# Kernel tuning notes

Hardware: AMD Instinct MI355X
Metric: run time of the kernel (lower is better)

The kernel has to match this reference:

```python
import jax, jax.numpy as jnp
import numpy as np

NUM_HEADS = 16
EPS = 1e-15


def setup_inputs() -> dict:
    key = jax.random.key(0)
    k1, k2, k3, k4 = jax.random.split(key, 4)
    B, N, C = 4, 16384, 512
    x = jax.random.normal(k1, (B, N, C), dtype=jnp.float32)
    qkv_weight = jax.random.normal(k2, (3 * C, C), dtype=jnp.float32) * 0.02
    proj_weight = jax.random.normal(k3, (C, C), dtype=jnp.float32) * 0.02
    proj_bias = jax.random.normal(k4, (C,), dtype=jnp.float32) * 0.02
    return {"x": x, "qkv_weight": qkv_weight, "proj_weight": proj_weight, "proj_bias": proj_bias}


def reference(x, qkv_weight, proj_weight, proj_bias):
    B, N, C = x.shape
    H = NUM_HEADS
    D = C // H
    # fused linear + ReLU on q,k (v stays linear, per backward: grad_v has no relu mask)
    qkv = (x @ qkv_weight.T).reshape(B, N, 3, C)
    q = jax.nn.relu(qkv[:, :, 0]).reshape(B, N, H, D)
    k = jax.nn.relu(qkv[:, :, 1]).reshape(B, N, H, D)
    v = qkv[:, :, 2].reshape(B, N, H, D)
    qf = q.astype(jnp.float32)
    kf = k.astype(jnp.float32)
    vf = v.astype(jnp.float32)
    # pad v with a ones column -> normalizer row in vk (pad_vk_mm_fwd)
    v_pad = jnp.concatenate([vf, jnp.ones_like(vf[..., :1])], axis=-1)  # [B,N,H,D+1]
    vk = jnp.einsum('bnhc,bnhd->bhcd', v_pad, kf)  # [B,H,D+1,D] accumulated in fp32
    vk_q = jnp.einsum('bnhd,bhcd->bnhc', qf, vk)  # [B,N,H,D+1]
    # fused division by normalizer (vk_q_mm_divide_fwd)
    proj_input = (vk_q[..., :-1] / (vk_q[..., -1:] + EPS)).astype(x.dtype).reshape(B, N, C)
    return proj_input @ proj_weight.T + proj_bias
```

## Files before the change

kernel.cpp:

```cpp
#include <hip/hip_runtime.h>
#include <stdint.h>

#define NB 4
#define SEQ 16384
#define CH 512
#define NH 16
#define HD 32
#define QKVC 1536
#define MROWS (NB * SEQ)

typedef unsigned short u16;
typedef __attribute__((ext_vector_type(8))) short bf16x8;
typedef __attribute__((ext_vector_type(4))) float f32x4;

__device__ __forceinline__ float bf2f(u16 u) {
  union { unsigned int i; float f; } c; c.i = ((unsigned int)u) << 16; return c.f;
}
__device__ __forceinline__ u16 f2bf(float f) {
  union { float f; unsigned int i; } c; c.f = f;
  return (u16)((c.i + 0x7fffu + ((c.i >> 16) & 1u)) >> 16);
}

__device__ __forceinline__ void async16(const u16* g, u16* l) {
  __builtin_amdgcn_global_load_lds((const __attribute__((address_space(1))) void*)g,
                                   (__attribute__((address_space(3))) void*)l,
                                   16, 0, 0);
}

__global__ void prep_kernel(const float* __restrict__ x,
                            const float* __restrict__ qw,
                            const float* __restrict__ pw,
                            u16* __restrict__ xb,
                            u16* __restrict__ qwb,
                            u16* __restrict__ pwb,
                            float* __restrict__ vk) {
  int gid = blockIdx.x * blockDim.x + threadIdx.x;
  int stride = gridDim.x * blockDim.x;

  const float4* x4 = (const float4*)x;
  ushort4* xb4 = (ushort4*)xb;
  for (int i = gid; i < (MROWS * CH / 4); i += stride) {
    float4 v = x4[i];
    ushort4 o; o.x = f2bf(v.x); o.y = f2bf(v.y); o.z = f2bf(v.z); o.w = f2bf(v.w);
    xb4[i] = o;
  }
  const float4* q4 = (const float4*)qw;
  ushort4* qwb4 = (ushort4*)qwb;
  for (int i = gid; i < (QKVC * CH / 4); i += stride) {
    float4 v = q4[i];
    ushort4 o; o.x = f2bf(v.x); o.y = f2bf(v.y); o.z = f2bf(v.z); o.w = f2bf(v.w);
    qwb4[i] = o;
  }
  const float4* p4 = (const float4*)pw;
  ushort4* pwb4 = (ushort4*)pwb;
  for (int i = gid; i < (CH * CH / 4); i += stride) {
    float4 v = p4[i];
    ushort4 o; o.x = f2bf(v.x); o.y = f2bf(v.y); o.z = f2bf(v.z); o.w = f2bf(v.w);
    pwb4[i] = o;
  }
  float4 z; z.x = 0.f; z.y = 0.f; z.z = 0.f; z.w = 0.f;
  float4* vk4 = (float4*)vk;
  for (int i = gid; i < (NB * NH * 33 * 32 / 4); i += stride) vk4[i] = z;
}

template <int N_DIM, bool RELU_QK, bool FINAL>
__global__ __launch_bounds__(512, 2) void gemm8p_kernel(
    const u16* __restrict__ A, const u16* __restrict__ Bm,
    void* __restrict__ Out, const float* __restrict__ bias) {
  __shared__ __align__(16) u16 lds[65536];

  const int tid = threadIdx.x;
  const int lane = tid & 63;
  const int w = tid >> 6;
  const int wr = w >> 2;
  const int wc = w & 3;
  const int fr = lane & 15;
  const int g = lane >> 4;
  const int xr = (fr & 7) << 3;

  const int gridX = N_DIM / 256;
  const int nwg = gridX * (MROWS / 256);
  int bid = blockIdx.y * gridX + blockIdx.x;
  bid = (bid & 7) * (nwg >> 3) + (bid >> 3);
  const long row0 = (long)(bid / gridX) * 256;
  const long col0 = (long)(bid % gridX) * 256;

  const int trow = tid >> 3;
  const int tcol = ((tid & 7) * 8) ^ (((tid >> 3) & 7) << 3);

#define STAGE_A(kt_, h_)                                                      \
  do {                                                                        \
    u16* lb_ = &lds[(((kt_) & 1) * 2 + (h_)) * 8192 + w * 512];               \
    const u16* ga_ = A + (size_t)(row0 + (h_) * 128 + trow) * 512 +           \
                     (kt_) * 64 + tcol;                                       \
    async16(ga_, lb_);                                                        \
    async16(ga_ + 64 * 512, lb_ + 4096);                                      \
  } while (0)

#define STAGE_B(kt_, h_)                                                      \
  do {                                                                        \
    u16* lb_ = &lds[32768 + (((kt_) & 1) * 2 + (h_)) * 8192 + w * 512];       \
    const u16* gb_ = Bm + (size_t)(col0 + (h_) * 128 + trow) * 512 +          \
                     (kt_) * 64 + tcol;                                       \
    async16(gb_, lb_);                                                        \
    async16(gb_ + 64 * 512, lb_ + 4096);                                      \
  } while (0)

  f32x4 acc[8][4];
#pragma unroll
  for (int m = 0; m < 8; m++)
#pragma unroll
    for (int n = 0; n < 4; n++) {
      f32x4 z = {0.f, 0.f, 0.f, 0.f};
      acc[m][n] = z;
    }
  bf16x8 a[4][2], b[4][2];

  STAGE_B(0, 0); STAGE_A(0, 0); STAGE_B(0, 1); STAGE_A(0, 1);
  STAGE_B(1, 0); STAGE_A(1, 0);
  asm volatile("s_waitcnt vmcnt(4)" ::: "memory");
  __builtin_amdgcn_s_barrier();

#pragma unroll
  for (int kt = 0; kt < 8; ++kt) {
    const int abase = ((kt & 1) * 2 + wr) * 8192;
    const int bbase = 32768 + ((kt & 1) * 2 + (wc >> 1)) * 8192 + (wc & 1) * 4096;

#pragma unroll
    for (int m = 0; m < 4; ++m)
#pragma unroll
      for (int kk = 0; kk < 2; ++kk)
        a[m][kk] = *(const bf16x8*)&lds[abase + (m * 16 + fr) * 64 + ((kk * 32 + g * 8) ^ xr)];
#pragma unroll
    for (int n = 0; n < 2; ++n)
#pragma unroll
      for (int kk = 0; kk < 2; ++kk)
        b[n][kk] = *(const bf16x8*)&lds[bbase + (n * 16 + fr) * 64 + ((kk * 32 + g * 8) ^ xr)];
    if (kt < 7) STAGE_B(kt + 1, 1);
    __builtin_amdgcn_s_barrier();
    asm volatile("s_waitcnt lgkmcnt(0)" ::: "memory");
    __builtin_amdgcn_s_setprio(1);
#pragma unroll
    for (int m = 0; m < 4; ++m)
#pragma unroll
      for (int n = 0; n < 2; ++n)
#pragma unroll
        for (int kk = 0; kk < 2; ++kk)
          acc[m][n] = __builtin_amdgcn_mfma_f32_16x16x32_bf16(a[m][kk], b[n][kk], acc[m][n], 0, 0, 0);
    __builtin_amdgcn_s_setprio(0);
    __builtin_amdgcn_s_barrier();

#pragma unroll
    for (int n = 0; n < 2; ++n)
#pragma unroll
      for (int kk = 0; kk < 2; ++kk)
        b[2 + n][kk] = *(const bf16x8*)&lds[bbase + ((n + 2) * 16 + fr) * 64 + ((kk * 32 + g * 8) ^ xr)];
    if (kt < 7) STAGE_A(kt + 1, 1);
    __builtin_amdgcn_s_barrier();
    asm volatile("s_waitcnt lgkmcnt(0)" ::: "memory");
    __builtin_amdgcn_s_setprio(1);
#pragma unroll
    for (int m = 0; m < 4; ++m)
#pragma unroll
      for (int n = 0; n < 2; ++n)
#pragma unroll
        for (int kk = 0; kk < 2; ++kk)
          acc[m][2 + n] = __builtin_amdgcn_mfma_f32_16x16x32_bf16(a[m][kk], b[2 + n][kk], acc[m][2 + n], 0, 0, 0);
    __builtin_amdgcn_s_setprio(0);
    __builtin_amdgcn_s_barrier();

#pragma unroll
    for (int m = 0; m < 4; ++m)
#pragma unroll
      for (int kk = 0; kk < 2; ++kk)
        a[m][kk] = *(const bf16x8*)&lds[abase + ((m + 4) * 16 + fr) * 64 + ((kk * 32 + g * 8) ^ xr)];
    if (kt < 6) STAGE_B(kt + 2, 0);
    __builtin_amdgcn_s_barrier();
    asm volatile("s_waitcnt lgkmcnt(0)" ::: "memory");
    __builtin_amdgcn_s_setprio(1);
#pragma unroll
    for (int m = 0; m < 4; ++m)
#pragma unroll
      for (int n = 0; n < 2; ++n)
#pragma unroll
        for (int kk = 0; kk < 2; ++kk)
          acc[4 + m][2 + n] = __builtin_amdgcn_mfma_f32_16x16x32_bf16(a[m][kk], b[2 + n][kk], acc[4 + m][2 + n], 0, 0, 0);
    __builtin_amdgcn_s_setprio(0);
    __builtin_amdgcn_s_barrier();

    if (kt < 6) {
      STAGE_A(kt + 2, 0);
      asm volatile("s_waitcnt vmcnt(4)" ::: "memory");
    } else {
      asm volatile("s_waitcnt vmcnt(0)" ::: "memory");
    }
    __builtin_amdgcn_s_barrier();
    __builtin_amdgcn_s_setprio(1);
#pragma unroll
    for (int m = 0; m < 4; ++m)
#pragma unroll
      for (int n = 0; n < 2; ++n)
#pragma unroll
        for (int kk = 0; kk < 2; ++kk)
          acc[4 + m][n] = __builtin_amdgcn_mfma_f32_16x16x32_bf16(a[m][kk], b[n][kk], acc[4 + m][n], 0, 0, 0);
    __builtin_amdgcn_s_setprio(0);
    __builtin_amdgcn_s_barrier();
  }
#undef STAGE_A
#undef STAGE_B

  const long rbase = row0 + wr * 128;
  const long cbase = col0 + wc * 64;
#pragma unroll
  for (int m = 0; m < 8; ++m)
#pragma unroll
    for (int n = 0; n < 4; ++n)
#pragma unroll
      for (int j = 0; j < 4; ++j) {
        long gr = rbase + m * 16 + g * 4 + j;
        long gc = cbase + n * 16 + fr;
        float v = acc[m][n][j];
        if constexpr (FINAL) {
          ((float*)Out)[gr * N_DIM + gc] = v + bias[gc];
        } else {
          if (RELU_QK && gc < 1024) v = fmaxf(v, 0.f);
          ((u16*)Out)[gr * N_DIM + gc] = f2bf(v);
        }
      }
}

__global__ __launch_bounds__(256) void vk_kernel(const u16* __restrict__ qkv,
                                                 float* __restrict__ vk) {
  __shared__ u16 tile[4][64 * 64];
  __shared__ float red[1056];

  const int tid = threadIdx.x;
  const int lane = tid & 63;
  const int w = tid >> 6;

  for (int i = tid; i < 1056; i += 256) red[i] = 0.f;
  __syncthreads();

  const int bh = blockIdx.x >> 4;
  const int split = blockIdx.x & 15;
  const int b = bh >> 4, h = bh & 15;

  const int s = lane & 7;
  const int rl = lane >> 3;
  const size_t gbase = (size_t)b * SEQ * QKVC + 512 + (size_t)(s >> 2) * 512 +
                       h * 32 + (s & 3) * 8;

  f32x4 acc[2][2];
  f32x4 accs[2];
#pragma unroll
  for (int tc = 0; tc < 2; tc++) {
    f32x4 z = {0.f, 0.f, 0.f, 0.f};
    accs[tc] = z;
#pragma unroll
    for (int td = 0; td < 2; td++) acc[tc][td] = z;
  }
  bf16x8 ones;
#pragma unroll
  for (int j = 0; j < 8; j++) ones[j] = (short)0x3F80;

  const int m = lane & 15;
  const int g = lane >> 4;
  u16* tw = tile[w];
  const int n0w = split * 1024 + w * 256;

  for (int t = 0; t < 4; ++t) {
    const int nt = n0w + t * 64;
#pragma unroll
    for (int p = 0; p < 8; ++p)
      async16(qkv + gbase + (size_t)(nt + p * 8 + rl) * QKVC, &tw[p * 512]);
    asm volatile("s_waitcnt vmcnt(0)" ::: "memory");
#pragma unroll
    for (int kk = 0; kk < 2; ++kk) {
      bf16x8 av[2], bk[2];
#pragma unroll
      for (int tc = 0; tc < 2; tc++)
#pragma unroll
        for (int j = 0; j < 8; j++)
          av[tc][j] = (short)tw[(kk * 32 + g * 8 + j) * 64 + 32 + tc * 16 + m];
#pragma unroll
      for (int td = 0; td < 2; td++)
#pragma unroll
        for (int j = 0; j < 8; j++)
          bk[td][j] = (short)tw[(kk * 32 + g * 8 + j) * 64 + td * 16 + m];
#pragma unroll
      for (int tc = 0; tc < 2; tc++)
#pragma unroll
        for (int td = 0; td < 2; td++)
          acc[tc][td] = __builtin_amdgcn_mfma_f32_16x16x32_bf16(av[tc], bk[td], acc[tc][td], 0, 0, 0);
#pragma unroll
      for (int td = 0; td < 2; td++)
        accs[td] = __builtin_amdgcn_mfma_f32_16x16x32_bf16(ones, bk[td], accs[td], 0, 0, 0);
    }
  }

#pragma unroll
  for (int tc = 0; tc < 2; tc++)
#pragma unroll
    for (int td = 0; td < 2; td++)
#pragma unroll
      for (int j = 0; j < 4; j++)
        atomicAdd(&red[(tc * 16 + g * 4 + j) * 32 + td * 16 + m], acc[tc][td][j]);
  if (lane < 16) {
#pragma unroll
    for (int td = 0; td < 2; td++)
      atomicAdd(&red[1024 + td * 16 + lane], accs[td][0]);
  }
  __syncthreads();
  float* dst = vk + (size_t)bh * 1056;
  for (int i = tid; i < 1056; i += 256) atomicAdd(&dst[i], red[i]);
}

__global__ __launch_bounds__(256) void vkq_kernel(const u16* __restrict__ qkv,
                                                  const float* __restrict__ vk,
                                                  u16* __restrict__ pi) {
  __shared__ float vkl[8 * 1056];
  __shared__ u16 ob[32 * 256];

  const int tid = threadIdx.x;
  const int chunk = blockIdx.x & 511;
  const int hh = (blockIdx.x >> 9) & 1;
  const int b = blockIdx.x >> 10;
  const int n0 = chunk * 32;

  const float* vg = vk + (size_t)(b * NH + hh * 8) * 1056;
  for (int i = tid; i < 8 * 1056; i += 256) vkl[i] = vg[i];
  __syncthreads();

  const int nl = tid & 31;
  const int hl = tid >> 5;
  const float* vkh = &vkl[hl * 1056];

  const u16* qp = qkv + ((size_t)b * SEQ + n0 + nl) * QKVC + (hh * 8 + hl) * 32;
  float qf[32];
#pragma unroll
  for (int s2 = 0; s2 < 4; ++s2) {
    bf16x8 qv = *(const bf16x8*)(qp + s2 * 8);
#pragma unroll
    for (int j = 0; j < 8; ++j) qf[s2 * 8 + j] = bf2f((u16)qv[j]);
  }

  float num[32];
#pragma unroll
  for (int c = 0; c < 32; ++c) {
    float a = 0.f;
#pragma unroll
    for (int d4 = 0; d4 < 8; ++d4) {
      f32x4 vv = *(const f32x4*)&vkh[c * 32 + d4 * 4];
      a = fmaf(qf[d4 * 4 + 0], vv[0], a);
      a = fmaf(qf[d4 * 4 + 1], vv[1], a);
      a = fmaf(qf[d4 * 4 + 2], vv[2], a);
      a = fmaf(qf[d4 * 4 + 3], vv[3], a);
    }
    num[c] = a;
  }
  float den = 0.f;
#pragma unroll
  for (int d4 = 0; d4 < 8; ++d4) {
    f32x4 vv = *(const f32x4*)&vkh[32 * 32 + d4 * 4];
    den = fmaf(qf[d4 * 4 + 0], vv[0], den);
    den = fmaf(qf[d4 * 4 + 1], vv[1], den);
    den = fmaf(qf[d4 * 4 + 2], vv[2], den);
    den = fmaf(qf[d4 * 4 + 3], vv[3], den);
  }
  const float r = 1.0f / (den + 1e-15f);
#pragma unroll
  for (int c = 0; c < 32; ++c) ob[nl * 256 + hl * 32 + c] = f2bf(num[c] * r);
  __syncthreads();

  u16* pg = pi + ((size_t)b * SEQ + n0) * CH + hh * 256;
  for (int i = tid; i < 1024; i += 256) {
    const int n = i >> 5;
    const int u = i & 31;
    *(bf16x8*)(pg + (size_t)n * CH + u * 8) = *(const bf16x8*)&ob[i * 8];
  }
}

extern "C" void kernel_launch(void* const* d_in, const int* in_sizes, int n_in,
                              void* d_out, int out_size, void* d_ws, size_t ws_size,
                              hipStream_t stream) {
  const float* x = (const float*)d_in[0];
  const float* qw = (const float*)d_in[1];
  const float* pw = (const float*)d_in[2];
  const float* bias = (const float*)d_in[3];

  char* ws = (char*)d_ws;
  u16* qkv = (u16*)(ws);
  u16* xb = (u16*)(ws + 201326592);
  u16* qwb = (u16*)(ws + 268435456);
  u16* pwb = (u16*)(ws + 270008320);
  float* vk = (float*)(ws + 270532608);
  u16* pi = xb;

  prep_kernel<<<2048, 256, 0, stream>>>(x, qw, pw, xb, qwb, pwb, vk);
  gemm8p_kernel<QKVC, true, false>
      <<<dim3(QKVC / 256, MROWS / 256), 512, 0, stream>>>(xb, qwb, qkv, nullptr);
  vk_kernel<<<NB * NH * 16, 256, 0, stream>>>(qkv, vk);
  vkq_kernel<<<NB * 2 * (SEQ / 32), 256, 0, stream>>>(qkv, vk, pi);
  gemm8p_kernel<CH, false, true>
      <<<dim3(CH / 256, MROWS / 256), 512, 0, stream>>>(pi, pwb, d_out, bias);
}
```

Baseline: 319.4 us.

## Make GEMM persistent over column tiles and move vk·q onto MFMA with split-bf16

The GEMM now launches one workgroup per 256-row block, and each workgroup loops over all column tiles with a fused k-loop. The A tile is re-read from L2 per column tile, and the epilogue stores each output tile inside the loop before resetting the accumulators. The vk·q kernel switches from scalar fp32 FMAs to bf16 MFMA, splitting vk into hi and lo bf16 parts to keep close to fp32 accuracy. The normaliser is computed by an extra padded MFMA and broadcast with a shuffle. Risks: lower parallelism with only 256 workgroups, and scalar per-element stores in the vkq output.

```diff
diff --git a/kernel.cpp b/kernel.cpp
--- a/kernel.cpp
+++ b/kernel.cpp
@@ -67,6 +67,8 @@
 __global__ __launch_bounds__(512, 2) void gemm8p_kernel(
     const u16* __restrict__ A, const u16* __restrict__ Bm,
     void* __restrict__ Out, const float* __restrict__ bias) {
+  constexpr int NT = N_DIM / 256;
+  constexpr int NKT = NT * 8;
   __shared__ __align__(16) u16 lds[65536];
 
   const int tid = threadIdx.x;
@@ -78,32 +80,33 @@
   const int g = lane >> 4;
   const int xr = (fr & 7) << 3;
 
-  const int gridX = N_DIM / 256;
-  const int nwg = gridX * (MROWS / 256);
-  int bid = blockIdx.y * gridX + blockIdx.x;
-  bid = (bid & 7) * (nwg >> 3) + (bid >> 3);
-  const long row0 = (long)(bid / gridX) * 256;
-  const long col0 = (long)(bid % gridX) * 256;
+  int bid = blockIdx.x;
+  bid = (bid & 7) * 32 + (bid >> 3);
+  const long row0 = (long)bid * 256;
 
   const int trow = tid >> 3;
   const int tcol = ((tid & 7) * 8) ^ (((tid >> 3) & 7) << 3);
 
-#define STAGE_A(kt_, h_)                                                      \
+#define STAGE_A(ktf_, h_)                                                     \
   do {                                                                        \
-    u16* lb_ = &lds[(((kt_) & 1) * 2 + (h_)) * 8192 + w * 512];               \
-    const u16* ga_ = A + (size_t)(row0 + (h_) * 128 + trow) * 512 +           \
-                     (kt_) * 64 + tcol;                                       \
-    async16(ga_, lb_);                                                        \
-    async16(ga_ + 64 * 512, lb_ + 4096);                                      \
+    if ((ktf_) < NKT) {                                                       \
+      u16* lb_ = &lds[(((ktf_) & 1) * 2 + (h_)) * 8192 + w * 512];            \
+      const u16* ga_ = A + (size_t)(row0 + (h_) * 128 + trow) * 512 +         \
+                       ((ktf_) & 7) * 64 + tcol;                              \
+      async16(ga_, lb_);                                                      \
+      async16(ga_ + 64 * 512, lb_ + 4096);                                    \
+    }                                                                         \
   } while (0)
 
-#define STAGE_B(kt_, h_)                                                      \
+#define STAGE_B(ktf_, h_)                                                     \
   do {                                                                        \
-    u16* lb_ = &lds[32768 + (((kt_) & 1) * 2 + (h_)) * 8192 + w * 512];       \
-    const u16* gb_ = Bm + (size_t)(col0 + (h_) * 128 + trow) * 512 +          \
-                     (kt_) * 64 + tcol;                                       \
-    async16(gb_, lb_);                                                        \
-    async16(gb_ + 64 * 512, lb_ + 4096);                                      \
+    if ((ktf_) < NKT) {                                                       \
+      u16* lb_ = &lds[32768 + (((ktf_) & 1) * 2 + (h_)) * 8192 + w * 512];    \
+      const u16* gb_ = Bm + (size_t)(((ktf_) >> 3) * 256 + (h_) * 128 +       \
+                                     trow) * 512 + ((ktf_) & 7) * 64 + tcol;  \
+      async16(gb_, lb_);                                                      \
+      async16(gb_ + 64 * 512, lb_ + 4096);                                    \
+    }                                                                         \
   } while (0)
 
   f32x4 acc[8][4];
@@ -121,10 +124,10 @@
   asm volatile("s_waitcnt vmcnt(4)" ::: "memory");
   __builtin_amdgcn_s_barrier();
 
-#pragma unroll
-  for (int kt = 0; kt < 8; ++kt) {
-    const int abase = ((kt & 1) * 2 + wr) * 8192;
-    const int bbase = 32768 + ((kt & 1) * 2 + (wc >> 1)) * 8192 + (wc & 1) * 4096;
+#pragma unroll 2
+  for (int ktf = 0; ktf < NKT; ++ktf) {
+    const int abase = ((ktf & 1) * 2 + wr) * 8192;
+    const int bbase = 32768 + ((ktf & 1) * 2 + (wc >> 1)) * 8192 + (wc & 1) * 4096;
 
 #pragma unroll
     for (int m = 0; m < 4; ++m)
@@ -136,7 +139,7 @@
 #pragma unroll
       for (int kk = 0; kk < 2; ++kk)
         b[n][kk] = *(const bf16x8*)&lds[bbase + (n * 16 + fr) * 64 + ((kk * 32 + g * 8) ^ xr)];
-    if (kt < 7) STAGE_B(kt + 1, 1);
+    STAGE_B(ktf + 1, 1);
     __builtin_amdgcn_s_barrier();
     asm volatile("s_waitcnt lgkmcnt(0)" ::: "memory");
     __builtin_amdgcn_s_setprio(1);
@@ -155,7 +158,7 @@
 #pragma unroll
       for (int kk = 0; kk < 2; ++kk)
         b[2 + n][kk] = *(const bf16x8*)&lds[bbase + ((n + 2) * 16 + fr) * 64 + ((kk * 32 + g * 8) ^ xr)];
-    if (kt < 7) STAGE_A(kt + 1, 1);
+    STAGE_A(ktf + 1, 1);
     __builtin_amdgcn_s_barrier();
     asm volatile("s_waitcnt lgkmcnt(0)" ::: "memory");
     __builtin_amdgcn_s_setprio(1);
@@ -174,7 +177,7 @@
 #pragma unroll
       for (int kk = 0; kk < 2; ++kk)
         a[m][kk] = *(const bf16x8*)&lds[abase + ((m + 4) * 16 + fr) * 64 + ((kk * 32 + g * 8) ^ xr)];
-    if (kt < 6) STAGE_B(kt + 2, 0);
+    STAGE_B(ktf + 2, 0);
     __builtin_amdgcn_s_barrier();
     asm volatile("s_waitcnt lgkmcnt(0)" ::: "memory");
     __builtin_amdgcn_s_setprio(1);
@@ -188,11 +191,11 @@
     __builtin_amdgcn_s_setprio(0);
     __builtin_amdgcn_s_barrier();
 
-    if (kt < 6) {
-      STAGE_A(kt + 2, 0);
+    STAGE_A(ktf + 2, 0);
+    if (ktf >= NKT - 2) {
+      asm volatile("s_waitcnt vmcnt(0)" ::: "memory");
+    } else {
       asm volatile("s_waitcnt vmcnt(4)" ::: "memory");
-    } else {
-      asm volatile("s_waitcnt vmcnt(0)" ::: "memory");
     }
     __builtin_amdgcn_s_barrier();
     __builtin_amdgcn_s_setprio(1);
@@ -205,28 +208,38 @@
           acc[4 + m][n] = __builtin_amdgcn_mfma_f32_16x16x32_bf16(a[m][kk], b[n][kk], acc[4 + m][n], 0, 0, 0);
     __builtin_amdgcn_s_setprio(0);
     __builtin_amdgcn_s_barrier();
+
+    if ((ktf & 7) == 7) {
+      const long col0 = (long)(ktf >> 3) * 256;
+      const long rbase = row0 + wr * 128;
+      const long cbase = col0 + wc * 64;
+#pragma unroll
+      for (int m = 0; m < 8; ++m)
+#pragma unroll
+        for (int n = 0; n < 4; ++n)
+#pragma unroll
+          for (int j = 0; j < 4; ++j) {
+            long gr = rbase + m * 16 + g * 4 + j;
+            long gc = cbase + n * 16 + fr;
+            float v = acc[m][n][j];
+            if constexpr (FINAL) {
+              ((float*)Out)[gr * N_DIM + gc] = v + bias[gc];
+            } else {
+              if (RELU_QK && gc < 1024) v = fmaxf(v, 0.f);
+              ((u16*)Out)[gr * N_DIM + gc] = f2bf(v);
+            }
+          }
+#pragma unroll
+      for (int m = 0; m < 8; ++m)
+#pragma unroll
+        for (int n = 0; n < 4; ++n) {
+          f32x4 z = {0.f, 0.f, 0.f, 0.f};
+          acc[m][n] = z;
+        }
+    }
   }
 #undef STAGE_A
 #undef STAGE_B
-
-  const long rbase = row0 + wr * 128;
-  const long cbase = col0 + wc * 64;
-#pragma unroll
-  for (int m = 0; m < 8; ++m)
-#pragma unroll
-    for (int n = 0; n < 4; ++n)
-#pragma unroll
-      for (int j = 0; j < 4; ++j) {
-        long gr = rbase + m * 16 + g * 4 + j;
-        long gc = cbase + n * 16 + fr;
-        float v = acc[m][n][j];
-        if constexpr (FINAL) {
-          ((float*)Out)[gr * N_DIM + gc] = v + bias[gc];
-        } else {
-          if (RELU_QK && gc < 1024) v = fmaxf(v, 0.f);
-          ((u16*)Out)[gr * N_DIM + gc] = f2bf(v);
-        }
-      }
 }
 
 __global__ __launch_bounds__(256) void vk_kernel(const u16* __restrict__ qkv,
@@ -318,65 +331,63 @@
 __global__ __launch_bounds__(256) void vkq_kernel(const u16* __restrict__ qkv,
                                                   const float* __restrict__ vk,
                                                   u16* __restrict__ pi) {
-  __shared__ float vkl[8 * 1056];
-  __shared__ u16 ob[32 * 256];
+  __shared__ u16 bhi[NH * 33 * 34];
+  __shared__ u16 blo[NH * 33 * 34];
 
   const int tid = threadIdx.x;
-  const int chunk = blockIdx.x & 511;
-  const int hh = (blockIdx.x >> 9) & 1;
-  const int b = blockIdx.x >> 10;
-  const int n0 = chunk * 32;
-
-  const float* vg = vk + (size_t)(b * NH + hh * 8) * 1056;
-  for (int i = tid; i < 8 * 1056; i += 256) vkl[i] = vg[i];
+  const int b = blockIdx.x >> 8;
+  const int n0 = (blockIdx.x & 255) * 64;
+
+  const float* vg = vk + (size_t)b * NH * 1056;
+  for (int i = tid; i < NH * 1056; i += 256) {
+    int h = i / 1056;
+    int rem = i - h * 1056;
+    int c = rem >> 5, d = rem & 31;
+    float v = vg[i];
+    u16 hv = f2bf(v);
+    float lo = v - bf2f(hv);
+    int dst = h * (33 * 34) + c * 34 + d;
+    bhi[dst] = hv;
+    blo[dst] = f2bf(lo);
+  }
   __syncthreads();
 
-  const int nl = tid & 31;
-  const int hl = tid >> 5;
-  const float* vkh = &vkl[hl * 1056];
-
-  const u16* qp = qkv + ((size_t)b * SEQ + n0 + nl) * QKVC + (hh * 8 + hl) * 32;
-  float qf[32];
-#pragma unroll
-  for (int s2 = 0; s2 < 4; ++s2) {
-    bf16x8 qv = *(const bf16x8*)(qp + s2 * 8);
-#pragma unroll
-    for (int j = 0; j < 8; ++j) qf[s2 * 8 + j] = bf2f((u16)qv[j]);
-  }
-
-  float num[32];
-#pragma unroll
-  for (int c = 0; c < 32; ++c) {
-    float a = 0.f;
-#pragma unroll
-    for (int d4 = 0; d4 < 8; ++d4) {
-      f32x4 vv = *(const f32x4*)&vkh[c * 32 + d4 * 4];
-      a = fmaf(qf[d4 * 4 + 0], vv[0], a);
-      a = fmaf(qf[d4 * 4 + 1], vv[1], a);
-      a = fmaf(qf[d4 * 4 + 2], vv[2], a);
-      a = fmaf(qf[d4 * 4 + 3], vv[3], a);
-    }
-    num[c] = a;
-  }
-  float den = 0.f;
-#pragma unroll
-  for (int d4 = 0; d4 < 8; ++d4) {
-    f32x4 vv = *(const f32x4*)&vkh[32 * 32 + d4 * 4];
-    den = fmaf(qf[d4 * 4 + 0], vv[0], den);
-    den = fmaf(qf[d4 * 4 + 1], vv[1], den);
-    den = fmaf(qf[d4 * 4 + 2], vv[2], den);
-    den = fmaf(qf[d4 * 4 + 3], vv[3], den);
-  }
-  const float r = 1.0f / (den + 1e-15f);
-#pragma unroll
-  for (int c = 0; c < 32; ++c) ob[nl * 256 + hl * 32 + c] = f2bf(num[c] * r);
-  __syncthreads();
-
-  u16* pg = pi + ((size_t)b * SEQ + n0) * CH + hh * 256;
-  for (int i = tid; i < 1024; i += 256) {
-    const int n = i >> 5;
-    const int u = i & 31;
-    *(bf16x8*)(pg + (size_t)n * CH + u * 8) = *(const bf16x8*)&ob[i * 8];
+  const int lane = tid & 63;
+  const int w = tid >> 6;
+  const int fr = lane & 15;
+  const int g = lane >> 4;
+
+  const u16* qbase = qkv + ((size_t)b * SEQ + n0 + w * 16 + fr) * QKVC;
+  u16* pbase = pi + ((size_t)b * SEQ + n0 + w * 16 + g * 4) * CH;
+
+  for (int h = 0; h < NH; ++h) {
+    bf16x8 a = *(const bf16x8*)(qbase + h * 32 + g * 8);
+    const int tb = h * (33 * 34);
+    bf16x8 h0 = *(const bf16x8*)&bhi[tb + fr * 34 + g * 8];
+    bf16x8 l0 = *(const bf16x8*)&blo[tb + fr * 34 + g * 8];
+    bf16x8 h1 = *(const bf16x8*)&bhi[tb + (16 + fr) * 34 + g * 8];
+    bf16x8 l1 = *(const bf16x8*)&blo[tb + (16 + fr) * 34 + g * 8];
+    bf16x8 h2, l2;
+#pragma unroll
+    for (int j = 0; j < 8; ++j) { h2[j] = 0; l2[j] = 0; }
+    if (fr == 0) {
+      h2 = *(const bf16x8*)&bhi[tb + 32 * 34 + g * 8];
+      l2 = *(const bf16x8*)&blo[tb + 32 * 34 + g * 8];
+    }
+    f32x4 z = {0.f, 0.f, 0.f, 0.f};
+    f32x4 c0 = __builtin_amdgcn_mfma_f32_16x16x32_bf16(a, l0, z, 0, 0, 0);
+    c0 = __builtin_amdgcn_mfma_f32_16x16x32_bf16(a, h0, c0, 0, 0, 0);
+    f32x4 c1 = __builtin_amdgcn_mfma_f32_16x16x32_bf16(a, l1, z, 0, 0, 0);
+    c1 = __builtin_amdgcn_mfma_f32_16x16x32_bf16(a, h1, c1, 0, 0, 0);
+    f32x4 c2 = __builtin_amdgcn_mfma_f32_16x16x32_bf16(a, l2, z, 0, 0, 0);
+    c2 = __builtin_amdgcn_mfma_f32_16x16x32_bf16(a, h2, c2, 0, 0, 0);
+#pragma unroll
+    for (int j = 0; j < 4; ++j) {
+      float den = __shfl(c2[j], lane & 48);
+      float r = 1.0f / (den + 1e-15f);
+      pbase[(size_t)j * CH + h * 32 + fr] = f2bf(c0[j] * r);
+      pbase[(size_t)j * CH + h * 32 + 16 + fr] = f2bf(c1[j] * r);
+    }
   }
 }
 
@@ -397,10 +408,8 @@
   u16* pi = xb;
 
   prep_kernel<<<2048, 256, 0, stream>>>(x, qw, pw, xb, qwb, pwb, vk);
-  gemm8p_kernel<QKVC, true, false>
-      <<<dim3(QKVC / 256, MROWS / 256), 512, 0, stream>>>(xb, qwb, qkv, nullptr);
+  gemm8p_kernel<QKVC, true, false><<<256, 512, 0, stream>>>(xb, qwb, qkv, nullptr);
   vk_kernel<<<NB * NH * 16, 256, 0, stream>>>(qkv, vk);
-  vkq_kernel<<<NB * 2 * (SEQ / 32), 256, 0, stream>>>(qkv, vk, pi);
-  gemm8p_kernel<CH, false, true>
-      <<<dim3(CH / 256, MROWS / 256), 512, 0, stream>>>(pi, pwb, d_out, bias);
-}
+  vkq_kernel<<<NB * (SEQ / 64), 256, 0, stream>>>(qkv, vk, pi);
+  gemm8p_kernel<CH, false, true><<<256, 512, 0, stream>>>(pi, pwb, d_out, bias);
+}
```

Measured after the change: 338.2 us. +5.9%, slower.
